# Optimization experiments

Measured on AMD Instinct MI355X. Metric: run time of the kernel, lower is better.

Reference implementation:

```python
import jax, jax.numpy as jnp
import numpy as np

N = 100000   # nodes
E = 3200000  # edges (avg degree 32)
F = 128      # feature dim
K = 10       # propagation order (hardcoded in module)


def setup_inputs() -> dict:
    key = jax.random.key(0)
    k1, k2 = jax.random.split(key, 2)
    x = jax.random.normal(k1, (N, F), dtype=jnp.float32)
    edge_index = jax.random.randint(k2, (2, E), 0, N, dtype=jnp.int32)
    mf_weights = jnp.ones((1, K + 1, 1), dtype=jnp.float32)
    # coef_upd='none' with alpha=0.5 -> lap_coefs init = min(1/0.5, 1.0) = 1.0, frozen
    lap_coefs = jnp.ones((K + 1,), dtype=jnp.float32)
    return {"x": x, "mf_weights": mf_weights, "lap_coefs": lap_coefs,
            "edge_index": edge_index}


def reference(x, mf_weights, lap_coefs, edge_index):
    n = x.shape[0]
    row, col = edge_index[0], edge_index[1]
    # gcn_norm without self loops: deg over destination (col), symmetric norm
    deg = jax.ops.segment_sum(jnp.ones((edge_index.shape[1],), x.dtype), col,
                              num_segments=n)
    dinv = jnp.where(deg > 0, jax.lax.rsqrt(jnp.maximum(deg, 1.0)) * jnp.where(deg > 0, jnp.ones_like(deg), 0.0), 0.0)
    dinv = jnp.where(deg > 0, deg ** -0.5, 0.0)
    norm = dinv[row] * dinv[col]  # [E]

    def prop(h):  # out[col] += norm * h[row]  (scatter-add SpMM)
        return jax.ops.segment_sum(norm[:, None] * h[row], col, num_segments=n)

    # Chebyshev-like recurrence: An=2, Bn=0, Cn=-1 -> P_i = 2*prop(P_{i-1}) - P_{i-2}
    outs = [x, prop(x)]
    for i in range(2, K + 1):
        outs.append(2.0 * prop(outs[-1]) - outs[-2])

    # coef_outs[0] = P0/1 ; coef_outs[i] = lap_coefs[i-1]/1 * P_i (norm_weights all 1)
    coef = jnp.concatenate([jnp.ones((1,), x.dtype), lap_coefs[:K]])  # [K+1]
    stacked = jnp.stack(outs, axis=1)  # [N, K+1, F]
    ret = jnp.sum(stacked * coef[None, :, None] * mf_weights, axis=1)  # [N, F]
    return ret
```

## Files before the change

kernel.cpp:

```cpp
#include <hip/hip_runtime.h>
#include <hip/hip_bf16.h>
#include <hip/hip_fp16.h>

#define FDIM 128

typedef float f4 __attribute__((ext_vector_type(4)));


__global__ void degree_kernel(const int* __restrict__ col, int* __restrict__ deg, int E) {
    int e = blockIdx.x * blockDim.x + threadIdx.x;
    if (e < E) atomicAdd(&deg[col[e]], 1);
}

__global__ void dinv_kernel(const int* __restrict__ deg, float* __restrict__ dinv, int N) {
    int i = blockIdx.x * blockDim.x + threadIdx.x;
    if (i < N) {
        int d = deg[i];
        dinv[i] = (d > 0) ? rsqrtf((float)d) : 0.0f;
    }
}


__global__ void scan_blocks_kernel(const int* __restrict__ deg, int* __restrict__ rowptr,
                                   int* __restrict__ bsum, int N) {
    __shared__ int s[256];
    int t = threadIdx.x;
    int i = blockIdx.x * 256 + t;
    int v = (i < N) ? deg[i] : 0;
    s[t] = v;
    __syncthreads();
    for (int off = 1; off < 256; off <<= 1) {
        int add = (t >= off) ? s[t - off] : 0;
        __syncthreads();
        s[t] += add;
        __syncthreads();
    }
    if (i < N) rowptr[i] = s[t] - v;
    if (t == 255) bsum[blockIdx.x] = s[255];
}

__global__ void scan_bsums_kernel(int* __restrict__ bsum, int* __restrict__ boff, int nb) {
    __shared__ int s[512];
    int t = threadIdx.x;
    int v = (t < nb) ? bsum[t] : 0;
    s[t] = v;
    __syncthreads();
    for (int off = 1; off < 512; off <<= 1) {
        int add = (t >= off) ? s[t - off] : 0;
        __syncthreads();
        s[t] += add;
        __syncthreads();
    }
    if (t < nb) boff[t] = s[t] - v;
}

__global__ void add_offsets_kernel(int* __restrict__ rowptr, int* __restrict__ cursor,
                                   const int* __restrict__ boff, int N, int E) {
    int i = blockIdx.x * blockDim.x + threadIdx.x;
    if (i < N) {
        int v = rowptr[i] + boff[i >> 8];
        rowptr[i] = v;
        cursor[i] = v;
    }
    if (i == 0) rowptr[N] = E;
}


__global__ void place_kernel(const int* __restrict__ row, const int* __restrict__ col,
                             int* __restrict__ cursor, int* __restrict__ eidx, int E) {
    int e = blockIdx.x * blockDim.x + threadIdx.x;
    if (e < E) {
        int c = col[e];
        int pos = atomicAdd(&cursor[c], 1);
        eidx[pos] = row[e];
    }
}


__global__ void init_out_kernel(const float4* __restrict__ x, const float* __restrict__ mf,
                                const float* __restrict__ dinv,
                                float4* __restrict__ out, float4* __restrict__ hx, long n8) {
    long i = (long)blockIdx.x * blockDim.x + threadIdx.x;
    if (i < n8) {
        float w = mf[0];
        float4 a = x[2 * i];
        float4 b = x[2 * i + 1];
        out[2 * i]     = make_float4(w * a.x, w * a.y, w * a.z, w * a.w);
        out[2 * i + 1] = make_float4(w * b.x, w * b.y, w * b.z, w * b.w);
        float dv = dinv[i >> 4];
        __half2 h[4];
        h[0] = __floats2half2_rn(dv * a.x, dv * a.y);
        h[1] = __floats2half2_rn(dv * a.z, dv * a.w);
        h[2] = __floats2half2_rn(dv * b.x, dv * b.y);
        h[3] = __floats2half2_rn(dv * b.z, dv * b.w);
        hx[i] = *(const float4*)h;
    }
}


__global__ __launch_bounds__(256) void gather_prop_kernel(
        const int* __restrict__ eidx, const int* __restrict__ rowptr,
        const float* __restrict__ dinv,
        const __half* __restrict__ src, const float* __restrict__ prev2,
        float* __restrict__ tgt, __half* __restrict__ tgth, float* __restrict__ out,
        const float* __restrict__ mf, const float* __restrict__ lap,
        int i_coef, float scale, float beta, int N) {
    int wid = blockIdx.x * 4 + (threadIdx.x >> 6);
    if (wid >= N) return;
    int lane = threadIdx.x & 63;
    int g  = lane >> 4;
    int fl = lane & 15;
    int feoff = fl << 3;

    int begin = rowptr[wid];
    int end   = rowptr[wid + 1];

    float acc[8];
    #pragma unroll
    for (int j = 0; j < 8; ++j) acc[j] = 0.f;

    #pragma unroll 4
    for (int e0 = begin; e0 < end; e0 += 4) {
        int e = e0 + g;
        float wsel = 0.f;
        int idx = 0;
        if (e < end) {
            idx = eidx[e];
            wsel = 1.f;
        }
        f4 raw = *(const f4*)(src + ((long)idx << 7) + feoff);
        const __half2* h = (const __half2*)&raw;
        float2 f0 = __half22float2(h[0]);
        float2 f1 = __half22float2(h[1]);
        float2 f2 = __half22float2(h[2]);
        float2 f3 = __half22float2(h[3]);
        acc[0] += wsel * f0.x; acc[1] += wsel * f0.y;
        acc[2] += wsel * f1.x; acc[3] += wsel * f1.y;
        acc[4] += wsel * f2.x; acc[5] += wsel * f2.y;
        acc[6] += wsel * f3.x; acc[7] += wsel * f3.y;
    }

    #pragma unroll
    for (int j = 0; j < 8; ++j) {
        acc[j] += __shfl_xor(acc[j], 16, 64);
        acc[j] += __shfl_xor(acc[j], 32, 64);
    }

    if (g == 0) {
        float dv   = dinv[wid];
        float sdv  = scale * dv;
        float coef = mf[i_coef] * lap[i_coef - 1];
        long o = ((long)wid << 7) + feoff;
        float r[8];
        if (beta != 0.f) {
            f4 p0 = __builtin_nontemporal_load((const f4*)(prev2 + o));
            f4 p1 = __builtin_nontemporal_load((const f4*)(prev2 + o) + 1);
            r[0] = sdv * acc[0] + beta * p0.x;
            r[1] = sdv * acc[1] + beta * p0.y;
            r[2] = sdv * acc[2] + beta * p0.z;
            r[3] = sdv * acc[3] + beta * p0.w;
            r[4] = sdv * acc[4] + beta * p1.x;
            r[5] = sdv * acc[5] + beta * p1.y;
            r[6] = sdv * acc[6] + beta * p1.z;
            r[7] = sdv * acc[7] + beta * p1.w;
        } else {
            #pragma unroll
            for (int j = 0; j < 8; ++j) r[j] = sdv * acc[j];
        }
        f4 t0 = {r[0], r[1], r[2], r[3]};
        f4 t1 = {r[4], r[5], r[6], r[7]};
        __builtin_nontemporal_store(t0, (f4*)(tgt + o));
        __builtin_nontemporal_store(t1, (f4*)(tgt + o) + 1);
        if (tgth) {
            __half2 hh[4];
            hh[0] = __floats2half2_rn(dv * r[0], dv * r[1]);
            hh[1] = __floats2half2_rn(dv * r[2], dv * r[3]);
            hh[2] = __floats2half2_rn(dv * r[4], dv * r[5]);
            hh[3] = __floats2half2_rn(dv * r[6], dv * r[7]);
            __builtin_nontemporal_store(*(const f4*)hh, (f4*)(tgth + o));
        }
        f4 o0 = __builtin_nontemporal_load((const f4*)(out + o));
        f4 o1 = __builtin_nontemporal_load((const f4*)(out + o) + 1);
        o0.x += coef * r[0]; o0.y += coef * r[1]; o0.z += coef * r[2]; o0.w += coef * r[3];
        o1.x += coef * r[4]; o1.y += coef * r[5]; o1.z += coef * r[6]; o1.w += coef * r[7];
        __builtin_nontemporal_store(o0, (f4*)(out + o));
        __builtin_nontemporal_store(o1, (f4*)(out + o) + 1);
    }
}

extern "C" void kernel_launch(void* const* d_in, const int* in_sizes, int n_in,
                              void* d_out, int out_size, void* d_ws, size_t ws_size,
                              hipStream_t stream) {
    const float* x   = (const float*)d_in[0];
    const float* mf  = (const float*)d_in[1];
    const float* lap = (const float*)d_in[2];
    const int*   ei  = (const int*)d_in[3];
    float* out = (float*)d_out;

    const int  K  = in_sizes[1] - 1;
    const long NF = (long)in_sizes[0];
    const int  N  = (int)(NF / FDIM);
    const int  E  = in_sizes[3] / 2;
    const int* row = ei;
    const int* col = ei + E;

    char* wp = (char*)d_ws;
    float*  bufA   = (float*)wp;  wp += NF * sizeof(float);
    float*  bufB   = (float*)wp;  wp += NF * sizeof(float);
    __half* hbufA  = (__half*)wp; wp += NF * sizeof(__half);
    __half* hbufB  = (__half*)wp; wp += NF * sizeof(__half);
    int*    eidx   = (int*)wp;    wp += (size_t)E * sizeof(int);
    int*    rowptr = (int*)wp;    wp += (size_t)(N + 1) * sizeof(int);
    int*    cursor = (int*)wp;    wp += (size_t)N * sizeof(int);
    int*    deg    = (int*)wp;    wp += (size_t)N * sizeof(int);
    float*  dinv   = (float*)wp;  wp += (size_t)N * sizeof(float);
    int*    bsum   = (int*)wp;    wp += 512 * sizeof(int);
    int*    boff   = (int*)wp;    wp += 512 * sizeof(int);

    const int BT = 256;
    const long n8 = NF / 8;
    const int n8_blocks = (int)((n8 + BT - 1) / BT);
    const int e_blocks  = (E + BT - 1) / BT;
    const int n_blocks  = (N + BT - 1) / BT;

    hipMemsetAsync(deg, 0, (size_t)N * sizeof(int), stream);
    degree_kernel<<<e_blocks, BT, 0, stream>>>(col, deg, E);
    dinv_kernel<<<n_blocks, BT, 0, stream>>>(deg, dinv, N);
    scan_blocks_kernel<<<n_blocks, BT, 0, stream>>>(deg, rowptr, bsum, N);
    scan_bsums_kernel<<<1, 512, 0, stream>>>(bsum, boff, n_blocks);
    add_offsets_kernel<<<n_blocks, BT, 0, stream>>>(rowptr, cursor, boff, N, E);
    place_kernel<<<e_blocks, BT, 0, stream>>>(row, col, cursor, eidx, E);

    init_out_kernel<<<n8_blocks, BT, 0, stream>>>((const float4*)x, mf, dinv,
                                                  (float4*)out, (float4*)hbufB, n8);

    const int g_blocks = (N + 3) / 4;

    gather_prop_kernel<<<g_blocks, BT, 0, stream>>>(eidx, rowptr, dinv, hbufB, x,
                                                    bufA, hbufA, out, mf, lap,
                                                    1, 1.0f, 0.0f, N);
    for (int i = 2; i <= K; ++i) {
        const __half* srch  = (i % 2 == 0) ? hbufA : hbufB;
        float*        tgt   = (i % 2 == 0) ? bufB : bufA;
        __half*       tgth  = (i % 2 == 0) ? hbufB : hbufA;
        const float*  prev2 = (i == 2) ? x : (const float*)tgt;
        if (i == K) tgth = nullptr;
        gather_prop_kernel<<<g_blocks, BT, 0, stream>>>(eidx, rowptr, dinv, srch, prev2,
                                                        tgt, tgth, out, mf, lap,
                                                        i, 2.0f, -1.0f, N);
    }
}
```

Before: 1.875 ms.

## Partition degree and CSR placement atomics by node range per XCD

Replaces the one-thread-per-edge degree count and CSR placement kernels with grid-stride kernels. Each block group, selected by blockIdx modulo 8, handles only destination nodes in one eighth of the node range. The intent is to keep atomics on deg and cursor local to one XCD's L2 and avoid cross-die coherence traffic. In exchange every block group rescans the full col array, so col is read eight times.

```diff
diff --git a/kernel.cpp b/kernel.cpp
--- a/kernel.cpp
+++ b/kernel.cpp
@@ -7,9 +7,16 @@
 typedef float f4 __attribute__((ext_vector_type(4)));
 
 
-__global__ void degree_kernel(const int* __restrict__ col, int* __restrict__ deg, int E) {
-    int e = blockIdx.x * blockDim.x + threadIdx.x;
-    if (e < E) atomicAdd(&deg[col[e]], 1);
+__global__ __launch_bounds__(256) void degree_oct_kernel(
+        const int* __restrict__ col, int* __restrict__ deg, int N, int E, int M) {
+    int o = blockIdx.x & 7;
+    int j = blockIdx.x >> 3;
+    int lo = (int)(((long)o * N) >> 3);
+    int hi = (int)(((long)(o + 1) * N) >> 3);
+    for (int e = j * 256 + threadIdx.x; e < E; e += M * 256) {
+        int c = col[e];
+        if (c >= lo && c < hi) atomicAdd(&deg[c], 1);
+    }
 }
 
 __global__ void dinv_kernel(const int* __restrict__ deg, float* __restrict__ dinv, int N) {
@@ -66,13 +73,19 @@
 }
 
 
-__global__ void place_kernel(const int* __restrict__ row, const int* __restrict__ col,
-                             int* __restrict__ cursor, int* __restrict__ eidx, int E) {
-    int e = blockIdx.x * blockDim.x + threadIdx.x;
-    if (e < E) {
+__global__ __launch_bounds__(256) void place_oct_kernel(
+        const int* __restrict__ row, const int* __restrict__ col,
+        int* __restrict__ cursor, int* __restrict__ eidx, int N, int E, int M) {
+    int o = blockIdx.x & 7;
+    int j = blockIdx.x >> 3;
+    int lo = (int)(((long)o * N) >> 3);
+    int hi = (int)(((long)(o + 1) * N) >> 3);
+    for (int e = j * 256 + threadIdx.x; e < E; e += M * 256) {
         int c = col[e];
-        int pos = atomicAdd(&cursor[c], 1);
-        eidx[pos] = row[e];
+        if (c >= lo && c < hi) {
+            int pos = atomicAdd(&cursor[c], 1);
+            eidx[pos] = row[e];
+        }
     }
 }
 
@@ -220,16 +233,16 @@
     const int BT = 256;
     const long n8 = NF / 8;
     const int n8_blocks = (int)((n8 + BT - 1) / BT);
-    const int e_blocks  = (E + BT - 1) / BT;
     const int n_blocks  = (N + BT - 1) / BT;
+    const int M = 192;
 
     hipMemsetAsync(deg, 0, (size_t)N * sizeof(int), stream);
-    degree_kernel<<<e_blocks, BT, 0, stream>>>(col, deg, E);
+    degree_oct_kernel<<<8 * M, BT, 0, stream>>>(col, deg, N, E, M);
     dinv_kernel<<<n_blocks, BT, 0, stream>>>(deg, dinv, N);
     scan_blocks_kernel<<<n_blocks, BT, 0, stream>>>(deg, rowptr, bsum, N);
     scan_bsums_kernel<<<1, 512, 0, stream>>>(bsum, boff, n_blocks);
     add_offsets_kernel<<<n_blocks, BT, 0, stream>>>(rowptr, cursor, boff, N, E);
-    place_kernel<<<e_blocks, BT, 0, stream>>>(row, col, cursor, eidx, E);
+    place_oct_kernel<<<8 * M, BT, 0, stream>>>(row, col, cursor, eidx, N, E, M);
 
     init_out_kernel<<<n8_blocks, BT, 0, stream>>>((const float4*)x, mf, dinv,
                                                   (float4*)out, (float4*)hbufB, n8);
```

Measured after the change: 1.753 ms. 1.07x faster.
